# Kernel optimization log

Hardware: AMD Instinct MI355X
Metric: run time of the kernel (lower is better)

Reference implementation:

```python
import jax, jax.numpy as jnp
import numpy as np
from jax.scipy.special import logsumexp

B, T, D = 16, 512, 768
S, H, O = 4, 48, 48
EMISS_W = 0.5  # args.emiss_nn_weight


def setup_inputs() -> dict:
    key = jax.random.key(0)
    ks = jax.random.split(key, 6)
    emb = jax.random.normal(ks[0], (B, T, D), jnp.float32)
    # obs must be valid per-source distributions over n_obs (log is taken)
    obs = jax.nn.softmax(2.0 * jax.random.normal(ks[1], (B, T, S, O), jnp.float32), axis=-1)
    # default prior init: priors = 0.001, priors[0] = 1, param = log(priors)
    p = jnp.full((H,), 0.001, jnp.float32).at[0].set(1.0)
    state_priors = jnp.log(p)
    unnorm_trans = jax.random.normal(ks[2], (H, H), jnp.float32)
    unnorm_emiss = jnp.zeros((S, H, O), jnp.float32)
    # xavier_uniform with relu gain for the per-source emission Linears
    bound = np.sqrt(2.0) * np.sqrt(6.0 / (D + H * O))
    W_emiss = jax.random.uniform(ks[3], (S, H * O, D), jnp.float32, -bound, bound)
    b_emiss = jnp.zeros((S, H * O), jnp.float32)
    seq_lengths = jax.random.randint(ks[4], (B,), T // 2, T + 1).astype(jnp.int32)
    seq_lengths = seq_lengths.at[0].set(T)  # max length == T
    return dict(emb=emb, obs=obs, state_priors=state_priors, unnorm_trans=unnorm_trans,
                unnorm_emiss=unnorm_emiss, W_emiss=W_emiss, b_emiss=b_emiss,
                seq_lengths=seq_lengths)


def _lognorm(x):
    return x - logsumexp(x, axis=-1, keepdims=True)


def reference(emb, obs, state_priors, unnorm_trans, unnorm_emiss, W_emiss, b_emiss, seq_lengths):
    lp = jax.nn.log_softmax(state_priors)                 # [H]
    log_trans = jax.nn.log_softmax(unnorm_trans, axis=-1)  # [H,H] (constant over b,t)
    emiss = jax.nn.softmax(unnorm_emiss, axis=-1)          # [S,H,O]

    # neural emissions: per-source Linear(d_emb -> H*O), softmax over O
    logits = jnp.einsum('btd,sod->btso', emb, W_emiss) + b_emiss  # [B,T,S,H*O]
    nn_emiss = jax.nn.softmax(logits.reshape(B, T, S, H, O), axis=-1)
    # (nn_trans is computed by NeuralModule in the original but discarded)

    log_emiss = jnp.log((1.0 - EMISS_W) * emiss[None, None] + EMISS_W * nn_emiss)  # [B,T,S,H,O]
    # log_matmul over obs axis, then sum over sources -> [B,T,H]
    lep = logsumexp(log_emiss + jnp.log(obs)[:, :, :, None, :], axis=-1).sum(axis=2)

    # forward recursion (normalized each step)
    a0 = _lognorm(lp + lep[:, 0])                          # [B,H]

    def fstep(a_prev, lep_t):
        a = _lognorm(lep_t + logsumexp(a_prev[:, :, None] + log_trans[None], axis=1))
        return a, a

    _, alphas = jax.lax.scan(fstep, a0, jnp.swapaxes(lep[:, 1:], 0, 1))
    log_alpha = jnp.concatenate([a0[:, None], jnp.swapaxes(alphas, 0, 1)], axis=1)  # [B,T,H]

    # backward recursion: beta[t] = logsumexp_j(trans[i,j] + lep[t,j] + beta[t+1,j])
    bT = jnp.zeros((B, H), lep.dtype)

    def bstep(b_next, lep_t):
        b = logsumexp(log_trans[None] + (lep_t + b_next)[:, None, :], axis=2)
        return b, b

    _, betas = jax.lax.scan(bstep, bT, jnp.swapaxes(lep[:, :T - 1], 0, 1), reverse=True)
    log_beta = jnp.concatenate([jnp.swapaxes(betas, 0, 1), bT[:, None]], axis=1)  # [B,T,H]
    # per-example roll by (length - T) along time, as in the original
    log_beta = jax.vmap(lambda b, s: jnp.roll(b, s, axis=0))(log_beta, seq_lengths - T)

    log_gamma = _lognorm(log_alpha + log_beta)             # [B,T,H]

    # xi_t = trans + alpha[t-1] (outer-sum) (lep[t] + beta[t]),  t = 1..T-1
    xi = (log_trans[None, None]
          + log_alpha[:, :-1, :, None]
          + (lep[:, 1:] + log_beta[:, 1:])[:, :, None, :])  # [B,T-1,H,H]
    xi = xi - logsumexp(xi, axis=(-2, -1), keepdims=True)

    log_prior = jnp.mean(jnp.sum(jnp.exp(log_gamma[:, 0]) * lp, axis=-1))

    tran_terms = jnp.sum(jnp.exp(xi) * log_trans[None, None], axis=(-2, -1))  # [B,T-1]
    mask_tr = (jnp.arange(T - 1)[None] < (seq_lengths - 1)[:, None]).astype(lep.dtype)
    log_tran = jnp.mean(jnp.sum(tran_terms * mask_tr, axis=1))

    emis_terms = jnp.sum(jnp.exp(log_gamma) * lep, axis=-1)  # [B,T]
    mask_em = (jnp.arange(T)[None] < seq_lengths[:, None]).astype(lep.dtype)
    log_emis = jnp.mean(jnp.sum(emis_terms * mask_em, axis=1))

    return log_prior + log_tran + log_emis
```

## Files before the change

kernel.cpp:

```cpp
#include <hip/hip_runtime.h>
#include <math.h>

namespace {

constexpr int Bn = 16, Tn = 512, Dn = 768, Sn = 4, Hn = 48, On = 48;
constexpr int Mn = Bn * Tn;
constexpr int Gn = Sn * Hn;
constexpr int Nn = Gn * On;
constexpr float EMISS_W = 0.5f;

constexpr size_t OFF_LP   = 0;
constexpr size_t OFF_LT   = 64;
constexpr size_t OFF_PT   = OFF_LT + Hn*Hn;
constexpr size_t OFF_EM   = OFF_PT + Hn*Hn;
constexpr size_t OFF_LEPP = OFF_EM + (size_t)Sn*Hn*On;
constexpr size_t OFF_LA   = OFF_LEPP + (size_t)Mn*Gn;
constexpr size_t OFF_LB   = OFF_LA + (size_t)Mn*Hn;
constexpr size_t OFF_RED  = OFF_LB + (size_t)Mn*Hn;
constexpr size_t FLOATS_END = OFF_RED + (size_t)Mn;

typedef __attribute__((ext_vector_type(8))) short short8;
typedef __attribute__((ext_vector_type(4))) float f32x4;

__device__ inline float waveSum(float v){
#pragma unroll
  for (int o = 32; o; o >>= 1) v += __shfl_xor(v, o);
  return v;
}

__device__ inline unsigned short f2bf(float f){
  unsigned int u = __float_as_uint(f);
  u += 0x7FFFu + ((u >> 16) & 1u);
  return (unsigned short)(u >> 16);
}

__device__ inline void gload_lds16(const void* g, void* l){
  __builtin_amdgcn_global_load_lds(
      (const __attribute__((address_space(1))) void*)g,
      (__attribute__((address_space(3))) void*)l, 16, 0, 0);
}

__global__ void convprep_kernel(const float* __restrict__ srcA, unsigned short* __restrict__ dstA,
                                int n4a,
                                const float* __restrict__ srcB, unsigned short* __restrict__ dstB,
                                int n4b,
                                const float* __restrict__ sp, const float* __restrict__ ut,
                                const float* __restrict__ ue, float* __restrict__ ws,
                                int nconv){
  const int tid = threadIdx.x;
  if ((int)blockIdx.x == nconv){
    float m = -INFINITY;
    for (int h = 0; h < Hn; ++h) m = fmaxf(m, sp[h]);
    float s = 0.f;
    for (int h = 0; h < Hn; ++h) s += __expf(sp[h] - m);
    float lse = m + __logf(s);
    if (tid < Hn) ws[OFF_LP + tid] = sp[tid] - lse;
    if (tid < Hn){
      const float* row = ut + tid * Hn;
      float mm = -INFINITY;
      for (int j = 0; j < Hn; ++j) mm = fmaxf(mm, row[j]);
      float ss = 0.f;
      for (int j = 0; j < Hn; ++j) ss += __expf(row[j] - mm);
      float l = mm + __logf(ss);
      for (int j = 0; j < Hn; ++j){
        float v = row[j] - l;
        ws[OFF_LT + tid*Hn + j] = v;
        ws[OFF_PT + tid*Hn + j] = __expf(v);
      }
    }
    for (int r = tid; r < Sn*Hn; r += blockDim.x){
      const float* row = ue + (size_t)r * On;
      float mm = -INFINITY;
      for (int o = 0; o < On; ++o) mm = fmaxf(mm, row[o]);
      float ss = 0.f;
      for (int o = 0; o < On; ++o) ss += __expf(row[o] - mm);
      float inv = 1.f/ss;
      for (int o = 0; o < On; ++o) ws[OFF_EM + (size_t)r*On + o] = __expf(row[o]-mm)*inv;
    }
    return;
  }
  int i = blockIdx.x * blockDim.x + tid;
  const float* s2; unsigned short* d; int k;
  if (i < n4a){ s2 = srcA; d = dstA; k = i; }
  else { k = i - n4a; if (k >= n4b) return; s2 = srcB; d = dstB; }
  float4 v = ((const float4*)s2)[k];
  ushort4 r;
  r.x = f2bf(v.x); r.y = f2bf(v.y); r.z = f2bf(v.z); r.w = f2bf(v.w);
  ((ushort4*)d)[k] = r;
}

constexpr int BM = 256, BN = 192, BK = 64;
constexpr int NKT = Dn / BK;

#define GEMM_BAR()  asm volatile("s_barrier" ::: "memory")
#define GEMM_LGKM() asm volatile("s_waitcnt lgkmcnt(0)" ::: "memory")

__global__ __launch_bounds__(512, 2) void gemm_lep_kernel(
    const unsigned short* __restrict__ embB, const unsigned short* __restrict__ WB,
    const float* __restrict__ bm, const float* __restrict__ obs,
    float* __restrict__ ws){
  __shared__ __align__(16) char smem[114688];
  __shared__ float bias_s[192], em_s[192];
  const int tid = threadIdx.x, lane = tid & 63, w = tid >> 6;
  const int bid = blockIdx.y * (Mn/BM) + blockIdx.x;
  const int xcd = bid & 7, j_loc = bid >> 3;
  const int xm = xcd & 3, xn = xcd >> 2;
  const int mloc = j_loc & 7, nloc = j_loc >> 3;
  const int m0 = (xm*8 + mloc) * BM;
  const int by = xn*24 + nloc;
  const int N0 = by * BN;
  if (tid < 192){
    bias_s[tid] = bm[N0 + tid];
    em_s[tid]   = ws[OFF_EM + N0 + tid];
  }
  const int wm = w & 1, wn = w >> 1;
  const int lm = lane & 15, q = lane >> 4;
  const int key = lm & 7;
  const int srow = lane >> 3, spc = lane & 7;
  const int aoff0 = (q ^ key) << 4;
  const int aoff1 = ((4 + q) ^ key) << 4;

  f32x4 acc[8][3];
#pragma unroll
  for (int i = 0; i < 8; ++i)
#pragma unroll
    for (int j = 0; j < 3; ++j) acc[i][j] = (f32x4){0.f,0.f,0.f,0.f};

  auto stageA2 = [&](int kt, int rb){
    const int r0  = rb + w*8;
    const int row = r0 + srow;
    const int lc  = spc ^ (row & 7);
    gload_lds16(embB + (size_t)(m0+row)*Dn + kt*BK + lc*8,
                smem + ((kt & 1) << 15) + r0*128);
  };
  auto stageB = [&](int kt, int i){
    const int idx = w*3 + i;
    const int row = idx*8 + srow;
    const int lc  = spc ^ (row & 7);
    gload_lds16(WB + (size_t)(N0+row)*Dn + kt*BK + lc*8,
                smem + 65536 + (kt & 1)*24576 + idx*1024);
  };

  stageA2(0,0); stageA2(0,64); stageA2(0,128); stageA2(0,192);
  stageB(0,0);  stageB(0,1);   stageB(0,2);
  asm volatile("s_waitcnt vmcnt(0)" ::: "memory");
  GEMM_BAR();

  for (int kt = 0; kt < NKT; ++kt){
    const char* Ab = smem + ((kt & 1) << 15);
    const char* Bb = smem + 65536 + (kt & 1)*24576;
    const int pf = kt + 1;
    const bool dopf = pf < NKT;
    short8 af[4], bf[3];

#pragma unroll
    for (int j = 0; j < 3; ++j)
      bf[j] = *(const short8*)(Bb + (wn*48 + j*16 + lm)*128 + aoff0);
#pragma unroll
    for (int i = 0; i < 4; ++i)
      af[i] = *(const short8*)(Ab + (wm*128 + i*16 + lm)*128 + aoff0);
    if (dopf){ stageA2(pf, 0); stageA2(pf, 64); }
    GEMM_BAR();
    GEMM_LGKM();
    __builtin_amdgcn_s_setprio(1);
#pragma unroll
    for (int i = 0; i < 4; ++i)
#pragma unroll
      for (int j = 0; j < 3; ++j)
        acc[i][j] = __builtin_amdgcn_mfma_f32_16x16x32_bf16(af[i], bf[j], acc[i][j], 0, 0, 0);
    __builtin_amdgcn_s_setprio(0);
    GEMM_BAR();

#pragma unroll
    for (int i = 0; i < 4; ++i)
      af[i] = *(const short8*)(Ab + (wm*128 + (4+i)*16 + lm)*128 + aoff0);
    if (dopf){ stageA2(pf, 128); stageA2(pf, 192); stageB(pf, 0); }
    GEMM_BAR();
    GEMM_LGKM();
    __builtin_amdgcn_s_setprio(1);
#pragma unroll
    for (int i = 0; i < 4; ++i)
#pragma unroll
      for (int j = 0; j < 3; ++j)
        acc[4+i][j] = __builtin_amdgcn_mfma_f32_16x16x32_bf16(af[i], bf[j], acc[4+i][j], 0, 0, 0);
    __builtin_amdgcn_s_setprio(0);
    GEMM_BAR();

#pragma unroll
    for (int j = 0; j < 3; ++j)
      bf[j] = *(const short8*)(Bb + (wn*48 + j*16 + lm)*128 + aoff1);
#pragma unroll
    for (int i = 0; i < 4; ++i)
      af[i] = *(const short8*)(Ab + (wm*128 + i*16 + lm)*128 + aoff1);
    if (dopf){ stageB(pf, 1); stageB(pf, 2); }
    GEMM_BAR();
    GEMM_LGKM();
    __builtin_amdgcn_s_setprio(1);
#pragma unroll
    for (int i = 0; i < 4; ++i)
#pragma unroll
      for (int j = 0; j < 3; ++j)
        acc[i][j] = __builtin_amdgcn_mfma_f32_16x16x32_bf16(af[i], bf[j], acc[i][j], 0, 0, 0);
    __builtin_amdgcn_s_setprio(0);
    GEMM_BAR();

#pragma unroll
    for (int i = 0; i < 4; ++i)
      af[i] = *(const short8*)(Ab + (wm*128 + (4+i)*16 + lm)*128 + aoff1);
    GEMM_BAR();
    GEMM_LGKM();
    __builtin_amdgcn_s_setprio(1);
#pragma unroll
    for (int i = 0; i < 4; ++i)
#pragma unroll
      for (int j = 0; j < 3; ++j)
        acc[4+i][j] = __builtin_amdgcn_mfma_f32_16x16x32_bf16(af[i], bf[j], acc[4+i][j], 0, 0, 0);
    __builtin_amdgcn_s_setprio(0);
    asm volatile("s_waitcnt vmcnt(0)" ::: "memory");
    GEMM_BAR();
  }

  float* Cp = (float*)smem;
#pragma unroll
  for (int h = 0; h < 2; ++h){
    if (h) __syncthreads();
#pragma unroll
    for (int i = 0; i < 4; ++i)
#pragma unroll
      for (int j = 0; j < 3; ++j){
        const int col = wn*48 + j*16 + lm;
#pragma unroll
        for (int r = 0; r < 4; ++r){
          const int rowl = wm*64 + i*16 + q*4 + r;
          Cp[rowl*193 + col] = acc[h*4+i][j][r];
        }
      }
    __syncthreads();
    {
      const int rowl = tid >> 2, grp = tid & 3;
      const int trow = (rowl >> 6)*128 + h*64 + (rowl & 63);
      const int m = m0 + trow;
      const int g = by*4 + grp;
      const int s2 = g / Hn;
      const float* crow = Cp + rowl*193 + grp*48;
      const float* ob   = obs + ((size_t)m*Sn + s2)*On;
      const float* bi   = bias_s + grp*48;
      const float* em   = em_s + grp*48;
      float Z = 0.f, pd = 0.f, eo = 0.f;
#pragma unroll
      for (int o = 0; o < On; ++o){
        float e = __expf(crow[o] + bi[o]);
        float obv = ob[o];
        Z += e;
        pd = fmaf(e, obv, pd);
        eo = fmaf(em[o], obv, eo);
      }
      ws[OFF_LEPP + (size_t)m*Gn + g] = __logf((1.f-EMISS_W)*eo + EMISS_W*(pd/Z));
    }
  }
}

constexpr int FBW = 24;
constexpr int FBL = 16;

__global__ __launch_bounds__(64) void fb_kernel(float* __restrict__ ws){
  __shared__ __align__(16) float ldsE[(FBW+FBL)*48];
  __shared__ __align__(16) float ring[2][64];
  const int lane = threadIdx.x;
  const int c    = blockIdx.x;
  const int b    = blockIdx.y;
  const bool fwd = blockIdx.z == 0;
  const bool act = lane < Hn;
  const int t0 = c*FBL, te = t0 + FBL - 1;

  float pt[Hn];
#pragma unroll
  for (int i = 0; i < Hn; ++i)
    pt[i] = act ? (fwd ? ws[OFF_PT + i*Hn + lane] : ws[OFF_PT + lane*Hn + i]) : 0.f;

  int row_lo, nrows, sA, sZ;
  bool exact;
  if (fwd){
    sA = t0 - FBW;
    exact = (sA < 1);
    row_lo = exact ? 0 : sA;
    if (exact) sA = 1;
    sZ = te;
    nrows = te - row_lo + 1;
  } else {
    int th = te + 1 + FBW;
    exact = (th > Tn - 2);
    sA = exact ? Tn - 2 : th - 1;
    sZ = t0;
    row_lo = t0;
    nrows = sA - t0 + 1;
  }

  {
    const float* src = ws + OFF_LEPP + ((size_t)b*Tn + row_lo)*Gn;
    int n4 = nrows * (Hn/4);
    for (int i = lane; i < n4; i += 64){
      int r = i / (Hn/4), h4 = i - r*(Hn/4);
      const float* p = src + (size_t)r*Gn + h4*4;
      float4 a = *(const float4*)(p);
      float4 b2 = *(const float4*)(p + Hn);
      float4 c2 = *(const float4*)(p + 2*Hn);
      float4 d2 = *(const float4*)(p + 3*Hn);
      float4 e;
      e.x = __expf(a.x + b2.x + c2.x + d2.x);
      e.y = __expf(a.y + b2.y + c2.y + d2.y);
      e.z = __expf(a.z + b2.z + c2.z + d2.z);
      e.w = __expf(a.w + b2.w + c2.w + d2.w);
      ((float4*)ldsE)[i] = e;
    }
  }
  __syncthreads();

  if (fwd){
    const size_t laF = OFF_LA + (size_t)b * Tn * Hn;
    float v;
    if (exact){
      v = act ? __expf(ws[OFF_LP + lane]) * ldsE[lane] : 0.f;
      if (c == 0 && act) ws[laF + lane] = v;
    } else {
      v = act ? 1.f : 0.f;
    }
    if (act) ring[0][lane] = v;
    __syncthreads();
    int cur = 0;
    for (int t = sA; t <= sZ; ++t){
      float S = waveSum(v);
      const float* rp = ring[cur];
      float s0=0.f,s1=0.f,s2=0.f,s3=0.f;
#pragma unroll
      for (int i = 0; i < Hn; i += 4){
        float4 a = *(const float4*)(rp + i);
        s0 = fmaf(a.x, pt[i+0], s0); s1 = fmaf(a.y, pt[i+1], s1);
        s2 = fmaf(a.z, pt[i+2], s2); s3 = fmaf(a.w, pt[i+3], s3);
      }
      float sd = (s0+s1)+(s2+s3);
      float e = act ? ldsE[(t - row_lo)*Hn + lane] : 0.f;
      float vn = act ? e * sd * (1.f/S) : 0.f;
      cur ^= 1;
      if (act) ring[cur][lane] = vn;
      __syncthreads();
      if (act && t >= t0) ws[laF + (size_t)t*Hn + lane] = vn;
      v = vn;
    }
  } else {
    const size_t lbF = OFF_LB + (size_t)b * Tn * Hn;
    float v = act ? 1.f : 0.f;
    if (exact && c == (Tn/FBL - 1) && act) ws[lbF + (size_t)(Tn-1)*Hn + lane] = 1.f;
    int cur = 0;
    for (int t = sA; t >= sZ; --t){
      float e = act ? ldsE[(t - row_lo)*Hn + lane] : 0.f;
      float wv = e * v;
      if (act) ring[cur][lane] = wv;
      float S = waveSum(wv);
      __syncthreads();
      const float* rp = ring[cur];
      float s0=0.f,s1=0.f,s2=0.f,s3=0.f;
#pragma unroll
      for (int j = 0; j < Hn; j += 4){
        float4 a = *(const float4*)(rp + j);
        s0 = fmaf(a.x, pt[j+0], s0); s1 = fmaf(a.y, pt[j+1], s1);
        s2 = fmaf(a.z, pt[j+2], s2); s3 = fmaf(a.w, pt[j+3], s3);
      }
      float vn = act ? ((s0+s1)+(s2+s3)) * (1.f/S) : 0.f;
      cur ^= 1;
      if (act && t <= te) ws[lbF + (size_t)t*Hn + lane] = vn;
      v = vn;
    }
  }
}

__global__ __launch_bounds__(256) void gamma_xi_kernel(
    const float* __restrict__ ws_c, float* __restrict__ ws,
    const int* __restrict__ seq_len){
  __shared__ float y_s[Hn], lap_s[Hn];
  __shared__ float red[8];
  const int tid = threadIdx.x;
  const int bid = blockIdx.x;
  const int b = bid >> 9, t = bid & (Tn-1);
  const int len = seq_len[b];
  int tb = t + (Tn - len); if (tb >= Tn) tb -= Tn;
  const size_t bt = (size_t)b*Tn + t;
  float lep = 0.f;
  if (tid < Hn){
    const float* lpp = ws_c + OFF_LEPP + bt*Gn + tid;
    lep = lpp[0] + lpp[Hn] + lpp[2*Hn] + lpp[3*Hn];
    float lb  = ws_c[OFF_LB + ((size_t)b*Tn + tb)*Hn + tid];
    y_s[tid] = __expf(lep) * lb;
    if (t >= 1) lap_s[tid] = ws_c[OFF_LA + (bt-1)*Hn + tid];
  }
  float emis_term = 0.f, prior_term = 0.f;
  if (tid < 64){
    int h = (tid < Hn) ? tid : 0;
    float la  = ws_c[OFF_LA + bt*Hn + h];
    float lb  = ws_c[OFF_LB + ((size_t)b*Tn + tb)*Hn + h];
    float lp  = ws_c[OFF_LP + h];
    float wgt = (tid < Hn) ? la*lb : 0.f;
    float Z = waveSum(wgt);
    float inv = 1.f / Z;
    emis_term  = waveSum(wgt * lep) * inv;
    prior_term = waveSum(wgt * lp) * inv;
  }
  __syncthreads();
  float tran_term = 0.f;
  if (t >= 1){
    float se = 0.f, st = 0.f;
#pragma unroll
    for (int k=0;k<9;++k){
      int e = tid + k*256;
      int i = e / Hn, j = e - i*Hn;
      float e2 = ws_c[OFF_PT + e] * lap_s[i] * y_s[j];
      se += e2;
      st = fmaf(e2, ws_c[OFF_LT + e], st);
    }
    se = waveSum(se);
    st = waveSum(st);
    const int wid = tid >> 6;
    if ((tid & 63) == 0){ red[wid] = se; red[4+wid] = st; }
    __syncthreads();
    if (tid == 0){
      float SE = red[0]+red[1]+red[2]+red[3];
      float ST = red[4]+red[5]+red[6]+red[7];
      tran_term = ST / SE;
    }
  }
  if (tid == 0){
    float tot = 0.f;
    if (t < len)            tot += emis_term;
    if (t == 0)             tot += prior_term;
    if (t >= 1 && t < len)  tot += tran_term;
    ws[OFF_RED + bid] = tot;
  }
}

__global__ __launch_bounds__(256) void sum_kernel(const float* __restrict__ ws,
                                                  float* __restrict__ out){
  __shared__ float red[4];
  const int tid = threadIdx.x;
  float s = 0.f;
  for (int i = tid; i < Mn; i += 256) s += ws[OFF_RED + i];
  s = waveSum(s);
  if ((tid & 63) == 0) red[tid >> 6] = s;
  __syncthreads();
  if (tid == 0) out[0] = (red[0]+red[1]+red[2]+red[3]) * (1.f / Bn);
}

}

extern "C" void kernel_launch(void* const* d_in, const int* in_sizes, int n_in,
                              void* d_out, int out_size, void* d_ws, size_t ws_size,
                              hipStream_t stream){
  const float* emb = (const float*)d_in[0];
  const float* obs = (const float*)d_in[1];
  const float* sp  = (const float*)d_in[2];
  const float* ut  = (const float*)d_in[3];
  const float* ue  = (const float*)d_in[4];
  const float* Wm  = (const float*)d_in[5];
  const float* bm  = (const float*)d_in[6];
  const int*   sl  = (const int*)d_in[7];
  float* ws  = (float*)d_ws;
  float* out = (float*)d_out;
  (void)in_sizes; (void)n_in; (void)ws_size; (void)out_size;

  unsigned short* embB = (unsigned short*)(ws + FLOATS_END);
  unsigned short* WB   = embB + (size_t)Mn * Dn;

  const int n4a = Mn*Dn/4, n4b = Nn*Dn/4;
  const int nconv = (n4a + n4b + 255)/256;
  convprep_kernel<<<nconv + 1, 256, 0, stream>>>(emb, embB, n4a, Wm, WB, n4b,
                                                 sp, ut, ue, ws, nconv);
  gemm_lep_kernel<<<dim3(Mn/BM, Nn/BN), 512, 0, stream>>>(embB, WB, bm, obs, ws);
  fb_kernel<<<dim3(Tn/FBL, Bn, 2), 64, 0, stream>>>(ws);
  gamma_xi_kernel<<<Bn*Tn, 256, 0, stream>>>(ws, ws, sl);
  sum_kernel<<<1, 256, 0, stream>>>(ws, out);
}
```

Measured before the change: 299.5 us.

## Shrink GEMM tile to 128x192 with 256 threads and reuse LDS for epilogue params

Halves the GEMM block tile in M (256 to 128) and drops to 4 waves per block, each wave now computing a 64x96 sub-tile (4x6 MFMA accumulators) instead of 128x48. This doubles the grid size, and shared memory per block falls from about 115KB to 80KB, which may allow more resident blocks per CU and better load balance. The bias and emission parameters are moved into the reused LDS region after the main loop rather than held in separate static arrays. The epilogue writes half the rows per pass, selected by which wave row owns them. Each block now loads the full B tile for a smaller M tile, so B traffic per unit of work doubles.

Result: no change. 294.5 us (-1.7%).

```diff
diff --git a/kernel.cpp b/kernel.cpp
--- a/kernel.cpp
+++ b/kernel.cpp
@@ -89,30 +89,25 @@
   ((ushort4*)d)[k] = r;
 }
 
-constexpr int BM = 256, BN = 192, BK = 64;
+constexpr int BM = 128, BN = 192, BK = 64;
 constexpr int NKT = Dn / BK;
 
 #define GEMM_BAR()  asm volatile("s_barrier" ::: "memory")
 #define GEMM_LGKM() asm volatile("s_waitcnt lgkmcnt(0)" ::: "memory")
 
-__global__ __launch_bounds__(512, 2) void gemm_lep_kernel(
+__global__ __launch_bounds__(256, 2) void gemm_lep_kernel(
     const unsigned short* __restrict__ embB, const unsigned short* __restrict__ WB,
     const float* __restrict__ bm, const float* __restrict__ obs,
     float* __restrict__ ws){
-  __shared__ __align__(16) char smem[114688];
-  __shared__ float bias_s[192], em_s[192];
+  __shared__ __align__(16) char smem[81920];
   const int tid = threadIdx.x, lane = tid & 63, w = tid >> 6;
   const int bid = blockIdx.y * (Mn/BM) + blockIdx.x;
   const int xcd = bid & 7, j_loc = bid >> 3;
   const int xm = xcd & 3, xn = xcd >> 2;
-  const int mloc = j_loc & 7, nloc = j_loc >> 3;
-  const int m0 = (xm*8 + mloc) * BM;
+  const int mloc = j_loc & 15, nloc = j_loc >> 4;
+  const int m0 = (xm*16 + mloc) * BM;
   const int by = xn*24 + nloc;
   const int N0 = by * BN;
-  if (tid < 192){
-    bias_s[tid] = bm[N0 + tid];
-    em_s[tid]   = ws[OFF_EM + N0 + tid];
-  }
   const int wm = w & 1, wn = w >> 1;
   const int lm = lane & 15, q = lane >> 4;
   const int key = lm & 7;
@@ -120,46 +115,49 @@
   const int aoff0 = (q ^ key) << 4;
   const int aoff1 = ((4 + q) ^ key) << 4;
 
-  f32x4 acc[8][3];
-#pragma unroll
-  for (int i = 0; i < 8; ++i)
-#pragma unroll
-    for (int j = 0; j < 3; ++j) acc[i][j] = (f32x4){0.f,0.f,0.f,0.f};
-
-  auto stageA2 = [&](int kt, int rb){
-    const int r0  = rb + w*8;
-    const int row = r0 + srow;
+  f32x4 acc[4][6];
+#pragma unroll
+  for (int i = 0; i < 4; ++i)
+#pragma unroll
+    for (int j = 0; j < 6; ++j) acc[i][j] = (f32x4){0.f,0.f,0.f,0.f};
+
+  auto stageA = [&](int kt, int i){
+    const int idx = w*4 + i;
+    const int row = idx*8 + srow;
     const int lc  = spc ^ (row & 7);
     gload_lds16(embB + (size_t)(m0+row)*Dn + kt*BK + lc*8,
-                smem + ((kt & 1) << 15) + r0*128);
+                smem + (kt & 1)*16384 + idx*1024);
   };
   auto stageB = [&](int kt, int i){
-    const int idx = w*3 + i;
+    const int idx = w*6 + i;
     const int row = idx*8 + srow;
     const int lc  = spc ^ (row & 7);
     gload_lds16(WB + (size_t)(N0+row)*Dn + kt*BK + lc*8,
-                smem + 65536 + (kt & 1)*24576 + idx*1024);
+                smem + 32768 + (kt & 1)*24576 + idx*1024);
   };
 
-  stageA2(0,0); stageA2(0,64); stageA2(0,128); stageA2(0,192);
-  stageB(0,0);  stageB(0,1);   stageB(0,2);
+#pragma unroll
+  for (int i = 0; i < 4; ++i) stageA(0, i);
+#pragma unroll
+  for (int i = 0; i < 6; ++i) stageB(0, i);
   asm volatile("s_waitcnt vmcnt(0)" ::: "memory");
   GEMM_BAR();
 
   for (int kt = 0; kt < NKT; ++kt){
-    const char* Ab = smem + ((kt & 1) << 15);
-    const char* Bb = smem + 65536 + (kt & 1)*24576;
+    const char* Ab = smem + (kt & 1)*16384;
+    const char* Bb = smem + 32768 + (kt & 1)*24576;
     const int pf = kt + 1;
     const bool dopf = pf < NKT;
     short8 af[4], bf[3];
 
 #pragma unroll
     for (int j = 0; j < 3; ++j)
-      bf[j] = *(const short8*)(Bb + (wn*48 + j*16 + lm)*128 + aoff0);
-#pragma unroll
-    for (int i = 0; i < 4; ++i)
-      af[i] = *(const short8*)(Ab + (wm*128 + i*16 + lm)*128 + aoff0);
-    if (dopf){ stageA2(pf, 0); stageA2(pf, 64); }
+      bf[j] = *(const short8*)(Bb + (wn*96 + j*16 + lm)*128 + aoff0);
+#pragma unroll
+    for (int i = 0; i < 4; ++i)
+      af[i] = *(const short8*)(Ab + (wm*64 + i*16 + lm)*128 + aoff0);
+    if (dopf){ stageA(pf,0); stageA(pf,1); stageA(pf,2); stageA(pf,3);
+               stageB(pf,0); stageB(pf,1); }
     GEMM_BAR();
     GEMM_LGKM();
     __builtin_amdgcn_s_setprio(1);
@@ -172,9 +170,9 @@
     GEMM_BAR();
 
 #pragma unroll
-    for (int i = 0; i < 4; ++i)
-      af[i] = *(const short8*)(Ab + (wm*128 + (4+i)*16 + lm)*128 + aoff0);
-    if (dopf){ stageA2(pf, 128); stageA2(pf, 192); stageB(pf, 0); }
+    for (int j = 0; j < 3; ++j)
+      bf[j] = *(const short8*)(Bb + (wn*96 + (3+j)*16 + lm)*128 + aoff0);
+    if (dopf){ stageB(pf,2); stageB(pf,3); }
     GEMM_BAR();
     GEMM_LGKM();
     __builtin_amdgcn_s_setprio(1);
@@ -182,17 +180,17 @@
     for (int i = 0; i < 4; ++i)
 #pragma unroll
       for (int j = 0; j < 3; ++j)
-        acc[4+i][j] = __builtin_amdgcn_mfma_f32_16x16x32_bf16(af[i], bf[j], acc[4+i][j], 0, 0, 0);
+        acc[i][3+j] = __builtin_amdgcn_mfma_f32_16x16x32_bf16(af[i], bf[j], acc[i][3+j], 0, 0, 0);
     __builtin_amdgcn_s_setprio(0);
     GEMM_BAR();
 
 #pragma unroll
     for (int j = 0; j < 3; ++j)
-      bf[j] = *(const short8*)(Bb + (wn*48 + j*16 + lm)*128 + aoff1);
-#pragma unroll
-    for (int i = 0; i < 4; ++i)
-      af[i] = *(const short8*)(Ab + (wm*128 + i*16 + lm)*128 + aoff1);
-    if (dopf){ stageB(pf, 1); stageB(pf, 2); }
+      bf[j] = *(const short8*)(Bb + (wn*96 + j*16 + lm)*128 + aoff1);
+#pragma unroll
+    for (int i = 0; i < 4; ++i)
+      af[i] = *(const short8*)(Ab + (wm*64 + i*16 + lm)*128 + aoff1);
+    if (dopf){ stageB(pf,4); stageB(pf,5); }
     GEMM_BAR();
     GEMM_LGKM();
     __builtin_amdgcn_s_setprio(1);
@@ -205,8 +203,8 @@
     GEMM_BAR();
 
 #pragma unroll
-    for (int i = 0; i < 4; ++i)
-      af[i] = *(const short8*)(Ab + (wm*128 + (4+i)*16 + lm)*128 + aoff1);
+    for (int j = 0; j < 3; ++j)
+      bf[j] = *(const short8*)(Bb + (wn*96 + (3+j)*16 + lm)*128 + aoff1);
     GEMM_BAR();
     GEMM_LGKM();
     __builtin_amdgcn_s_setprio(1);
@@ -214,38 +212,44 @@
     for (int i = 0; i < 4; ++i)
 #pragma unroll
       for (int j = 0; j < 3; ++j)
-        acc[4+i][j] = __builtin_amdgcn_mfma_f32_16x16x32_bf16(af[i], bf[j], acc[4+i][j], 0, 0, 0);
+        acc[i][3+j] = __builtin_amdgcn_mfma_f32_16x16x32_bf16(af[i], bf[j], acc[i][3+j], 0, 0, 0);
     __builtin_amdgcn_s_setprio(0);
     asm volatile("s_waitcnt vmcnt(0)" ::: "memory");
     GEMM_BAR();
   }
 
-  float* Cp = (float*)smem;
+  float* Cp  = (float*)smem;
+  float* ext = (float*)(smem + 49408);
+  if (tid < 192){
+    ext[tid]       = bm[N0 + tid];
+    ext[192 + tid] = ws[OFF_EM + N0 + tid];
+  }
 #pragma unroll
   for (int h = 0; h < 2; ++h){
     if (h) __syncthreads();
-#pragma unroll
-    for (int i = 0; i < 4; ++i)
-#pragma unroll
-      for (int j = 0; j < 3; ++j){
-        const int col = wn*48 + j*16 + lm;
-#pragma unroll
-        for (int r = 0; r < 4; ++r){
-          const int rowl = wm*64 + i*16 + q*4 + r;
-          Cp[rowl*193 + col] = acc[h*4+i][j][r];
+    if (wm == h){
+#pragma unroll
+      for (int i = 0; i < 4; ++i)
+#pragma unroll
+        for (int j = 0; j < 6; ++j){
+          const int col = wn*96 + j*16 + lm;
+#pragma unroll
+          for (int r = 0; r < 4; ++r){
+            const int rowl = i*16 + q*4 + r;
+            Cp[rowl*193 + col] = acc[i][j][r];
+          }
         }
-      }
+    }
     __syncthreads();
     {
       const int rowl = tid >> 2, grp = tid & 3;
-      const int trow = (rowl >> 6)*128 + h*64 + (rowl & 63);
-      const int m = m0 + trow;
+      const int m = m0 + h*64 + rowl;
       const int g = by*4 + grp;
       const int s2 = g / Hn;
       const float* crow = Cp + rowl*193 + grp*48;
       const float* ob   = obs + ((size_t)m*Sn + s2)*On;
-      const float* bi   = bias_s + grp*48;
-      const float* em   = em_s + grp*48;
+      const float* bi   = ext + grp*48;
+      const float* em   = ext + 192 + grp*48;
       float Z = 0.f, pd = 0.f, eo = 0.f;
 #pragma unroll
       for (int o = 0; o < On; ++o){
@@ -473,7 +477,7 @@
   const int nconv = (n4a + n4b + 255)/256;
   convprep_kernel<<<nconv + 1, 256, 0, stream>>>(emb, embB, n4a, Wm, WB, n4b,
                                                  sp, ut, ue, ws, nconv);
-  gemm_lep_kernel<<<dim3(Mn/BM, Nn/BN), 512, 0, stream>>>(embB, WB, bm, obs, ws);
+  gemm_lep_kernel<<<dim3(Mn/BM, Nn/BN), 256, 0, stream>>>(embB, WB, bm, obs, ws);
   fb_kernel<<<dim3(Tn/FBL, Bn, 2), 64, 0, stream>>>(ws);
   gamma_xi_kernel<<<Bn*Tn, 256, 0, stream>>>(ws, ws, sl);
   sum_kernel<<<1, 256, 0, stream>>>(ws, out);
```
